# Kernel tuning notes

Hardware: AMD Instinct MI355X
Metric: run time of the kernel (lower is better)

## Reference

```python
import jax, jax.numpy as jnp
import numpy as np

B, S, D_IN, D_E = 8, 2048, 1024, 1024


def setup_inputs() -> dict:
    key = jax.random.key(0)
    ks = jax.random.split(key, 9)
    s_in = 1.0 / np.sqrt(D_IN)
    s_e = 1.0 / np.sqrt(D_E)
    return {
        "x": jax.random.normal(ks[0], (B, S, D_IN), dtype=jnp.float32),
        "Wq": jax.random.uniform(ks[1], (D_IN, D_E), jnp.float32, -s_in, s_in),
        "bq": jax.random.uniform(ks[2], (D_E,), jnp.float32, -s_in, s_in),
        "Wk": jax.random.uniform(ks[3], (D_IN, D_E), jnp.float32, -s_in, s_in),
        "bk": jax.random.uniform(ks[4], (D_E,), jnp.float32, -s_in, s_in),
        "Wv": jax.random.uniform(ks[5], (D_IN, D_E), jnp.float32, -s_in, s_in),
        "bv": jax.random.uniform(ks[6], (D_E,), jnp.float32, -s_in, s_in),
        "Wo": jax.random.uniform(ks[7], (D_E, D_E), jnp.float32, -s_e, s_e),
        "bo": jax.random.uniform(ks[8], (D_E,), jnp.float32, -s_e, s_e),
    }


def reference(x, Wq, bq, Wk, bk, Wv, bv, Wo, bo):
    # QKV projections: [B,S,D_in] @ [D_in,D_e] -> [B,S,D_e]
    Q = jnp.einsum("bsi,ie->bse", x, Wq) + bq
    K = jnp.einsum("bsi,ie->bse", x, Wk) + bk
    V = jnp.einsum("bsi,ie->bse", x, Wv) + bv
    scale = 1.0 / jnp.sqrt(jnp.asarray(Q.shape[-1], Q.dtype))
    # full score matrix [B,S,S] (faithful to the unfused original)
    logits = jnp.einsum("bqe,bke->bqk", Q, K) * scale
    attn = jax.nn.softmax(logits, axis=-1)
    values = jnp.einsum("bqk,bke->bqe", attn, V)
    o = jnp.einsum("bqe,ef->bqf", values, Wo) + bo
    return o
```

## Files before the change

### kernel.cpp

```cpp
#include <hip/hip_runtime.h>

#define DIN 1024
#define DE  1024
#define SEQ 2048
#define NB  8

typedef __bf16 bf16x8 __attribute__((ext_vector_type(8)));
typedef float  f32x4  __attribute__((ext_vector_type(4)));
typedef unsigned short u16;
typedef u16 u16x8 __attribute__((ext_vector_type(8)));
typedef u16 u16x4 __attribute__((ext_vector_type(4)));

__device__ __forceinline__ u16 f2bf(float f) {
  unsigned u = __builtin_bit_cast(unsigned, f);
  return (u16)((u + 0x7FFFu + ((u >> 16) & 1u)) >> 16);
}
__device__ __forceinline__ float bf2f(u16 h) {
  return __builtin_bit_cast(float, (unsigned)h << 16);
}

typedef __attribute__((address_space(1))) const unsigned char g_u8;
typedef __attribute__((address_space(3))) unsigned char l_u8;
__device__ __forceinline__ void gload16(const void* g, void* l) {
  __builtin_amdgcn_global_load_lds((g_u8*)g, (l_u8*)l, 16, 0, 0);
}

__global__ __launch_bounds__(256) void cvt_f32_bf16(const float* __restrict__ in,
                                                    u16* __restrict__ out, int n4) {
  int i = blockIdx.x * 256 + threadIdx.x;
  if (i >= n4) return;
  float4 v = ((const float4*)in)[i];
  u16x4 o;
  o[0] = f2bf(v.x); o[1] = f2bf(v.y); o[2] = f2bf(v.z); o[3] = f2bf(v.w);
  ((u16x4*)out)[i] = o;
}

__global__ __launch_bounds__(256) void transpose_w(const float* __restrict__ W,
                                                   u16* __restrict__ Wt) {
  __shared__ float t[32][33];
  const int tx = threadIdx.x, ty = threadIdx.y;
  const int bx = blockIdx.x * 32, by = blockIdx.y * 32;
#pragma unroll
  for (int i = 0; i < 4; ++i)
    t[ty + i * 8][tx] = W[(size_t)(by + ty + i * 8) * 1024 + bx + tx];
  __syncthreads();
#pragma unroll
  for (int i = 0; i < 4; ++i)
    Wt[(size_t)(bx + ty + i * 8) * 1024 + by + tx] = f2bf(t[tx][ty + i * 8]);
}

__global__ __launch_bounds__(256) void softmax_rows_bf16(u16* __restrict__ P) {
  const size_t row = blockIdx.x;
  u16* pr = P + row * 2048 + (size_t)threadIdx.x * 8;
  u16x8 v = *(const u16x8*)pr;
  float x[8];
#pragma unroll
  for (int j = 0; j < 8; ++j) x[j] = bf2f(v[j]);
  float m = x[0];
#pragma unroll
  for (int j = 1; j < 8; ++j) m = fmaxf(m, x[j]);
#pragma unroll
  for (int off = 32; off; off >>= 1) m = fmaxf(m, __shfl_xor(m, off));
  __shared__ float rm[4], rs[4];
  const int lane = threadIdx.x & 63, wid = threadIdx.x >> 6;
  if (lane == 0) rm[wid] = m;
  __syncthreads();
  m = fmaxf(fmaxf(rm[0], rm[1]), fmaxf(rm[2], rm[3]));
  float s = 0.f;
#pragma unroll
  for (int j = 0; j < 8; ++j) { x[j] = __expf(x[j] - m); s += x[j]; }
#pragma unroll
  for (int off = 32; off; off >>= 1) s += __shfl_xor(s, off);
  if (lane == 0) rs[wid] = s;
  __syncthreads();
  s = (rs[0] + rs[1]) + (rs[2] + rs[3]);
  const float inv = 1.f / s;
  u16x8 o;
#pragma unroll
  for (int j = 0; j < 8; ++j) o[j] = f2bf(x[j] * inv);
  *(u16x8*)pr = o;
}

template <int BMT, int OMODE, bool HAS_BIAS>
__global__ __launch_bounds__(512, 1) void gemmph(
    const u16* __restrict__ A, const u16* __restrict__ Bt, void* __restrict__ Cv,
    const float* __restrict__ bias, int M, int N, int K,
    size_t sA, size_t sB, size_t sC, float scale) {
  constexpr int ABYTES = BMT * 128;
  constexpr int AHALF  = ABYTES / 2;
  constexpr int BUFB   = ABYTES + 32768;
  constexpr int LA     = AHALF / 8192;
  constexpr int MR     = BMT / 32;
  __shared__ __align__(16) char lds8[2 * BUFB];
  const int tid = threadIdx.x, lane = tid & 63, wid = tid >> 6;
  const int wm = wid >> 2, wn = wid & 3;
  const int lane15 = lane & 15, gk = lane >> 4;

  const int gx = gridDim.x, gy = gridDim.y;
  int lin = blockIdx.x + gx * (blockIdx.y + gy * blockIdx.z);
  const int nwg = gx * gy * (int)gridDim.z;
  const int q = nwg >> 3, r8 = nwg & 7;
  const int xcd = lin & 7, idx = lin >> 3;
  lin = (xcd < r8 ? xcd * (q + 1) : r8 * (q + 1) + (xcd - r8) * q) + idx;
  const int bz = lin / (gx * gy);
  const int rem = lin - bz * (gx * gy);
  const int by = rem / gx, bx = rem - (rem / gx) * gx;

  const char* Ag = (const char*)(A + (size_t)bz * sA + (size_t)by * BMT * K);
  const char* Bg = (const char*)(Bt + (size_t)bz * sB + (size_t)bx * 256 * K);
  const size_t Kb = (size_t)K * 2;

  const int spr = tid >> 3;
  const int sg = (tid & 7) ^ (spr & 7);
  const char* srcA[2][2];
  const char* srcB[2][2];
#pragma unroll
  for (int h = 0; h < 2; ++h) {
#pragma unroll
    for (int j = 0; j < LA; ++j)
      srcA[h][j] = Ag + (size_t)(h * (BMT / 2) + j * 64 + spr) * Kb + sg * 16;
#pragma unroll
    for (int j = 0; j < 2; ++j)
      srcB[h][j] = Bg + (size_t)(h * 128 + j * 64 + spr) * Kb + sg * 16;
  }

  auto stageA2 = [&](int dbuf) {
#pragma unroll
    for (int h = 0; h < 2; ++h) {
      char* d = lds8 + dbuf * BUFB + h * AHALF + tid * 16;
#pragma unroll
      for (int j = 0; j < LA; ++j) { gload16(srcA[h][j], d + j * 8192); srcA[h][j] += 128; }
    }
  };
  auto stageB1 = [&](int h, int dbuf) {
    char* d = lds8 + dbuf * BUFB + ABYTES + h * 16384 + tid * 16;
    gload16(srcB[h][0], d);        srcB[h][0] += 128;
    gload16(srcB[h][1], d + 8192); srcB[h][1] += 128;
  };

  const int arow = lane15 * 128 + ((gk ^ (lane15 & 7)) << 4);

  f32x4 acc[MR][4] = {};
  const int NT = K >> 6;

  stageA2(0); stageB1(0, 0); stageB1(1, 0);
  stageB1(0, 1); stageA2(1);
  if constexpr (BMT == 256) asm volatile("s_waitcnt vmcnt(6)" ::: "memory");
  else                      asm volatile("s_waitcnt vmcnt(4)" ::: "memory");
  __builtin_amdgcn_s_barrier();
  __builtin_amdgcn_sched_barrier(0);

  for (int kt = 0; kt < NT; ++kt) {
    const char* Ab = lds8 + (kt & 1) * BUFB + wm * AHALF;
    const char* Bb = lds8 + (kt & 1) * BUFB + ABYTES + (wn >> 1) * 16384 + (wn & 1) * 8192;
    const int nbuf = (kt + 1) & 1;
    const int cbuf = kt & 1;
    bf16x8 af[4][2], bfr[4][2];

    if constexpr (BMT == 256) {
#pragma unroll
      for (int m = 0; m < 4; ++m) {
        af[m][0] = *(const bf16x8*)(Ab + m * 2048 + arow);
        af[m][1] = *(const bf16x8*)(Ab + m * 2048 + (arow ^ 64));
      }
#pragma unroll
      for (int n = 0; n < 2; ++n) {
        bfr[n][0] = *(const bf16x8*)(Bb + n * 2048 + arow);
        bfr[n][1] = *(const bf16x8*)(Bb + n * 2048 + (arow ^ 64));
      }
      if (kt + 1 < NT) stageB1(1, nbuf);
      __builtin_amdgcn_s_barrier();
      asm volatile("s_waitcnt lgkmcnt(0)" ::: "memory");
      __builtin_amdgcn_sched_barrier(0);
      __builtin_amdgcn_s_setprio(1);
#pragma unroll
      for (int m = 0; m < 4; ++m)
#pragma unroll
        for (int n = 0; n < 2; ++n) {
          acc[m][n] = __builtin_amdgcn_mfma_f32_16x16x32_bf16(af[m][0], bfr[n][0], acc[m][n], 0, 0, 0);
          acc[m][n] = __builtin_amdgcn_mfma_f32_16x16x32_bf16(af[m][1], bfr[n][1], acc[m][n], 0, 0, 0);
        }
      __builtin_amdgcn_s_setprio(0);
      __builtin_amdgcn_s_barrier();
      __builtin_amdgcn_sched_barrier(0);
#pragma unroll
      for (int n = 2; n < 4; ++n) {
        bfr[n][0] = *(const bf16x8*)(Bb + n * 2048 + arow);
        bfr[n][1] = *(const bf16x8*)(Bb + n * 2048 + (arow ^ 64));
      }
      __builtin_amdgcn_s_barrier();
      asm volatile("s_waitcnt lgkmcnt(0)" ::: "memory");
      __builtin_amdgcn_sched_barrier(0);
      __builtin_amdgcn_s_setprio(1);
#pragma unroll
      for (int m = 0; m < 4; ++m)
#pragma unroll
        for (int n = 2; n < 4; ++n) {
          acc[m][n] = __builtin_amdgcn_mfma_f32_16x16x32_bf16(af[m][0], bfr[n][0], acc[m][n], 0, 0, 0);
          acc[m][n] = __builtin_amdgcn_mfma_f32_16x16x32_bf16(af[m][1], bfr[n][1], acc[m][n], 0, 0, 0);
        }
      __builtin_amdgcn_s_setprio(0);
      __builtin_amdgcn_s_barrier();
      __builtin_amdgcn_sched_barrier(0);
#pragma unroll
      for (int m = 0; m < 4; ++m) {
        af[m][0] = *(const bf16x8*)(Ab + (4 + m) * 2048 + arow);
        af[m][1] = *(const bf16x8*)(Ab + (4 + m) * 2048 + (arow ^ 64));
      }
      if (kt + 2 < NT) stageB1(0, cbuf);
      __builtin_amdgcn_s_barrier();
      asm volatile("s_waitcnt lgkmcnt(0)" ::: "memory");
      __builtin_amdgcn_sched_barrier(0);
      __builtin_amdgcn_s_setprio(1);
#pragma unroll
      for (int m = 0; m < 4; ++m)
#pragma unroll
        for (int n = 0; n < 2; ++n) {
          acc[4 + m][n] = __builtin_amdgcn_mfma_f32_16x16x32_bf16(af[m][0], bfr[n][0], acc[4 + m][n], 0, 0, 0);
          acc[4 + m][n] = __builtin_amdgcn_mfma_f32_16x16x32_bf16(af[m][1], bfr[n][1], acc[4 + m][n], 0, 0, 0);
        }
      __builtin_amdgcn_s_setprio(0);
      __builtin_amdgcn_s_barrier();
      __builtin_amdgcn_sched_barrier(0);
      if (kt + 2 < NT) stageA2(cbuf);
      __builtin_amdgcn_s_barrier();
      asm volatile("s_waitcnt lgkmcnt(0)" ::: "memory");
      __builtin_amdgcn_sched_barrier(0);
      __builtin_amdgcn_s_setprio(1);
#pragma unroll
      for (int m = 0; m < 4; ++m)
#pragma unroll
        for (int n = 2; n < 4; ++n) {
          acc[4 + m][n] = __builtin_amdgcn_mfma_f32_16x16x32_bf16(af[m][0], bfr[n][0], acc[4 + m][n], 0, 0, 0);
          acc[4 + m][n] = __builtin_amdgcn_mfma_f32_16x16x32_bf16(af[m][1], bfr[n][1], acc[4 + m][n], 0, 0, 0);
        }
      __builtin_amdgcn_s_setprio(0);
      if (kt < NT - 2)      asm volatile("s_waitcnt vmcnt(6)" ::: "memory");
      else if (kt == NT - 2) asm volatile("s_waitcnt vmcnt(0)" ::: "memory");
      __builtin_amdgcn_s_barrier();
      __builtin_amdgcn_sched_barrier(0);
    } else {
#pragma unroll
      for (int m = 0; m < 4; ++m) {
        af[m][0] = *(const bf16x8*)(Ab + m * 2048 + arow);
        af[m][1] = *(const bf16x8*)(Ab + m * 2048 + (arow ^ 64));
      }
#pragma unroll
      for (int n = 0; n < 4; ++n) {
        bfr[n][0] = *(const bf16x8*)(Bb + n * 2048 + arow);
        bfr[n][1] = *(const bf16x8*)(Bb + n * 2048 + (arow ^ 64));
      }
      if (kt + 1 < NT) stageB1(1, nbuf);
      __builtin_amdgcn_s_barrier();
      asm volatile("s_waitcnt lgkmcnt(0)" ::: "memory");
      __builtin_amdgcn_sched_barrier(0);
      __builtin_amdgcn_s_setprio(1);
#pragma unroll
      for (int m = 0; m < 4; ++m)
#pragma unroll
        for (int n = 0; n < 2; ++n) {
          acc[m][n] = __builtin_amdgcn_mfma_f32_16x16x32_bf16(af[m][0], bfr[n][0], acc[m][n], 0, 0, 0);
          acc[m][n] = __builtin_amdgcn_mfma_f32_16x16x32_bf16(af[m][1], bfr[n][1], acc[m][n], 0, 0, 0);
        }
      __builtin_amdgcn_s_setprio(0);
      __builtin_amdgcn_s_barrier();
      __builtin_amdgcn_sched_barrier(0);
      if (kt + 2 < NT) { stageA2(cbuf); stageB1(0, cbuf); }
      __builtin_amdgcn_s_barrier();
      asm volatile("s_waitcnt lgkmcnt(0)" ::: "memory");
      __builtin_amdgcn_sched_barrier(0);
      __builtin_amdgcn_s_setprio(1);
#pragma unroll
      for (int m = 0; m < 4; ++m)
#pragma unroll
        for (int n = 2; n < 4; ++n) {
          acc[m][n] = __builtin_amdgcn_mfma_f32_16x16x32_bf16(af[m][0], bfr[n][0], acc[m][n], 0, 0, 0);
          acc[m][n] = __builtin_amdgcn_mfma_f32_16x16x32_bf16(af[m][1], bfr[n][1], acc[m][n], 0, 0, 0);
        }
      __builtin_amdgcn_s_setprio(0);
      if (kt < NT - 2)      asm volatile("s_waitcnt vmcnt(4)" ::: "memory");
      else if (kt == NT - 2) asm volatile("s_waitcnt vmcnt(0)" ::: "memory");
      __builtin_amdgcn_s_barrier();
      __builtin_amdgcn_sched_barrier(0);
    }
  }

  const int rbase = by * BMT + wm * (BMT / 2) + (gk << 2);
  const int cbase = bx * 256 + wn * 64 + lane15;
#pragma unroll
  for (int m = 0; m < MR; ++m)
#pragma unroll
    for (int n = 0; n < 4; ++n) {
      const int col = cbase + n * 16;
      const float bval = HAS_BIAS ? bias[col] : 0.f;
#pragma unroll
      for (int r = 0; r < 4; ++r) {
        const int rowg = rbase + m * 16 + r;
        const float v = acc[m][n][r] * scale + bval;
        if (OMODE == 0)
          ((float*)Cv)[(size_t)bz * sC + (size_t)rowg * N + col] = v;
        else if (OMODE == 1)
          ((u16*)Cv)[(size_t)bz * sC + (size_t)rowg * N + col] = f2bf(v);
        else
          ((u16*)Cv)[(size_t)(rowg >> 11) * ((size_t)DE * SEQ) +
                     (size_t)col * SEQ + (rowg & 2047)] = f2bf(v);
      }
    }
}

extern "C" void kernel_launch(void* const* d_in, const int* in_sizes, int n_in,
                              void* d_out, int out_size, void* d_ws, size_t ws_size,
                              hipStream_t stream) {
  const float* x  = (const float*)d_in[0];
  const float* Wq = (const float*)d_in[1];
  const float* bq = (const float*)d_in[2];
  const float* Wk = (const float*)d_in[3];
  const float* bk = (const float*)d_in[4];
  const float* Wv = (const float*)d_in[5];
  const float* bv = (const float*)d_in[6];
  const float* Wo = (const float*)d_in[7];
  const float* bo = (const float*)d_in[8];

  const size_t NEED = 142606336;
  if (ws_size < NEED) return;
  char* ws = (char*)d_ws;
  u16* x_bf = (u16*)(ws);
  u16* q_bf = (u16*)(ws + 33554432);
  u16* k_bf = (u16*)(ws + 67108864);
  u16* vt   = (u16*)(ws + 100663296);
  u16* wt   = (u16*)(ws + 134217728);
  u16* lgP  = (u16*)d_out;
  u16* wt_q = wt;
  u16* wt_k = wt + 1048576;
  u16* wt_v = wt + 2097152;
  u16* wt_o = wt + 3145728;

  dim3 tb(32, 8);
  const size_t sQ = (size_t)SEQ * DE;
  const size_t sL = (size_t)SEQ * SEQ;

  cvt_f32_bf16<<<16384, 256, 0, stream>>>(x, x_bf, (NB * SEQ * DIN) / 4);
  transpose_w<<<dim3(32, 32), tb, 0, stream>>>(Wq, wt_q);
  transpose_w<<<dim3(32, 32), tb, 0, stream>>>(Wk, wt_k);
  transpose_w<<<dim3(32, 32), tb, 0, stream>>>(Wv, wt_v);
  transpose_w<<<dim3(32, 32), tb, 0, stream>>>(Wo, wt_o);
  gemmph<256, 1, true><<<dim3(4, 64, 1), 512, 0, stream>>>(x_bf, wt_q, q_bf, bq,
      16384, 1024, 1024, 0, 0, 0, 1.f);
  gemmph<256, 1, true><<<dim3(4, 64, 1), 512, 0, stream>>>(x_bf, wt_k, k_bf, bk,
      16384, 1024, 1024, 0, 0, 0, 1.f);
  gemmph<256, 2, true><<<dim3(4, 64, 1), 512, 0, stream>>>(x_bf, wt_v, vt, bv,
      16384, 1024, 1024, 0, 0, 0, 1.f);
  gemmph<256, 1, false><<<dim3(8, 8, 8), 512, 0, stream>>>(q_bf, k_bf, lgP,
      nullptr, 2048, 2048, 1024, sQ, sQ, sL, 0.03125f);
  softmax_rows_bf16<<<16384, 256, 0, stream>>>(lgP);
  gemmph<256, 1, false><<<dim3(4, 8, 8), 512, 0, stream>>>(lgP, vt, q_bf,
      nullptr, 2048, 1024, 2048, sL, sQ, sQ, 1.f);
  gemmph<256, 0, true><<<dim3(4, 64, 1), 512, 0, stream>>>(q_bf, wt_o, d_out, bo,
      16384, 1024, 1024, 0, 0, 0, 1.f);

  (void)in_sizes; (void)n_in; (void)out_size; (void)ws_size;
}
```

Before: 334.6 us.

## Add 256x128-tile batched GEMM kernel for attention score and PV products

```diff
diff --git a/kernel.cpp b/kernel.cpp
--- a/kernel.cpp
+++ b/kernel.cpp
@@ -79,6 +79,98 @@
 #pragma unroll
   for (int j = 0; j < 8; ++j) o[j] = f2bf(x[j] * inv);
   *(u16x8*)pr = o;
+}
+
+__global__ __launch_bounds__(256) void gemmcc(
+    const u16* __restrict__ A, const u16* __restrict__ Bt, u16* __restrict__ C,
+    int M, int N, int K, size_t sA, size_t sB, size_t sC, float scale) {
+  constexpr int BUF = 24576;
+  __shared__ __align__(16) char lds[2 * BUF];
+  const int tid = threadIdx.x, lane = tid & 63, wid = tid >> 6;
+  const int wm = wid >> 1, wn = wid & 1;
+  const int lane15 = lane & 15, gk = lane >> 4;
+
+  const int gx = gridDim.x, gy = gridDim.y;
+  int lin = blockIdx.x + gx * (blockIdx.y + gy * blockIdx.z);
+  const int nwg = gx * gy * (int)gridDim.z;
+  const int q = nwg >> 3, r8 = nwg & 7;
+  const int xcd = lin & 7, idx = lin >> 3;
+  lin = (xcd < r8 ? xcd * (q + 1) : r8 * (q + 1) + (xcd - r8) * q) + idx;
+  const int bz = lin / (gx * gy);
+  const int rem = lin - bz * (gx * gy);
+  const int by = rem / gx, bx = rem - (rem / gx) * gx;
+
+  const char* Ag = (const char*)(A + (size_t)bz * sA + (size_t)by * 256 * K);
+  const char* Bg = (const char*)(Bt + (size_t)bz * sB + (size_t)bx * 128 * K);
+  const size_t Kb = (size_t)K * 2;
+
+  const char* sa[4];
+  const char* sb[2];
+  int dA[4], dB[2];
+#pragma unroll
+  for (int j = 0; j < 4; ++j) {
+    const int ls = j * 256 + tid, pr = ls >> 2, ps = ls & 3;
+    sa[j] = Ag + (size_t)pr * Kb + (ps ^ ((pr >> 1) & 3)) * 16;
+    dA[j] = ls * 16;
+  }
+#pragma unroll
+  for (int j = 0; j < 2; ++j) {
+    const int ls = j * 256 + tid, pr = ls >> 2, ps = ls & 3;
+    sb[j] = Bg + (size_t)pr * Kb + (ps ^ ((pr >> 1) & 3)) * 16;
+    dB[j] = 16384 + ls * 16;
+  }
+  auto stage = [&](int b) {
+    char* base = lds + b * BUF;
+#pragma unroll
+    for (int j = 0; j < 4; ++j) { gload16(sa[j], base + dA[j]); sa[j] += 64; }
+#pragma unroll
+    for (int j = 0; j < 2; ++j) { gload16(sb[j], base + dB[j]); sb[j] += 64; }
+  };
+
+  const int sw = (gk ^ ((lane15 >> 1) & 3)) << 4;
+  const int aoffB = wm * 8192 + lane15 * 64 + sw;
+  const int boffB = 16384 + wn * 4096 + lane15 * 64 + sw;
+
+  f32x4 acc[8][4] = {};
+  const int NT = K >> 5;
+
+  stage(0);
+  asm volatile("s_waitcnt vmcnt(0)" ::: "memory");
+  __builtin_amdgcn_s_barrier();
+  __builtin_amdgcn_sched_barrier(0);
+
+  for (int t = 0; t < NT; ++t) {
+    if (t + 1 < NT) stage((t + 1) & 1);
+    const char* base = lds + (t & 1) * BUF;
+    bf16x8 af[8], bfv[4];
+#pragma unroll
+    for (int n = 0; n < 4; ++n) bfv[n] = *(const bf16x8*)(base + boffB + n * 1024);
+#pragma unroll
+    for (int m = 0; m < 8; ++m) af[m] = *(const bf16x8*)(base + aoffB + m * 1024);
+    __builtin_amdgcn_s_setprio(1);
+#pragma unroll
+    for (int m = 0; m < 8; ++m)
+#pragma unroll
+      for (int n = 0; n < 4; ++n)
+        acc[m][n] = __builtin_amdgcn_mfma_f32_16x16x32_bf16(af[m], bfv[n], acc[m][n], 0, 0, 0);
+    __builtin_amdgcn_s_setprio(0);
+    asm volatile("s_waitcnt vmcnt(0)" ::: "memory");
+    __builtin_amdgcn_s_barrier();
+    __builtin_amdgcn_sched_barrier(0);
+  }
+
+  const int rbase = by * 256 + wm * 128 + (gk << 2);
+  const int cbase = bx * 128 + wn * 64 + lane15;
+  u16* Cb = C + (size_t)bz * sC;
+#pragma unroll
+  for (int m = 0; m < 8; ++m)
+#pragma unroll
+    for (int n = 0; n < 4; ++n) {
+      const int col = cbase + n * 16;
+#pragma unroll
+      for (int r = 0; r < 4; ++r)
+        Cb[(size_t)(rbase + m * 16 + r) * N + col] = f2bf(acc[m][n][r] * scale);
+    }
 }
 
 template <int BMT, int OMODE, bool HAS_BIAS>
@@ -145,8 +237,7 @@
 
   stageA2(0); stageB1(0, 0); stageB1(1, 0);
   stageB1(0, 1); stageA2(1);
-  if constexpr (BMT == 256) asm volatile("s_waitcnt vmcnt(6)" ::: "memory");
-  else                      asm volatile("s_waitcnt vmcnt(4)" ::: "memory");
+  asm volatile("s_waitcnt vmcnt(6)" ::: "memory");
   __builtin_amdgcn_s_barrier();
   __builtin_amdgcn_sched_barrier(0);
 
@@ -157,132 +248,87 @@
     const int cbuf = kt & 1;
     bf16x8 af[4][2], bfr[4][2];
 
-    if constexpr (BMT == 256) {
-#pragma unroll
-      for (int m = 0; m < 4; ++m) {
-        af[m][0] = *(const bf16x8*)(Ab + m * 2048 + arow);
-        af[m][1] = *(const bf16x8*)(Ab + m * 2048 + (arow ^ 64));
+#pragma unroll
+    for (int m = 0; m < 4; ++m) {
+      af[m][0] = *(const bf16x8*)(Ab + m * 2048 + arow);
+      af[m][1] = *(const bf16x8*)(Ab + m * 2048 + (arow ^ 64));
+    }
+#pragma unroll
+    for (int n = 0; n < 2; ++n) {
+      bfr[n][0] = *(const bf16x8*)(Bb + n * 2048 + arow);
+      bfr[n][1] = *(const bf16x8*)(Bb + n * 2048 + (arow ^ 64));
+    }
+    if (kt + 1 < NT) stageB1(1, nbuf);
+    __builtin_amdgcn_s_barrier();
+    asm volatile("s_waitcnt lgkmcnt(0)" ::: "memory");
+    __builtin_amdgcn_sched_barrier(0);
+    __builtin_amdgcn_s_setprio(1);
+#pragma unroll
+    for (int m = 0; m < 4; ++m)
+#pragma unroll
+      for (int n = 0; n < 2; ++n) {
+        acc[m][n] = __builtin_amdgcn_mfma_f32_16x16x32_bf16(af[m][0], bfr[n][0], acc[m][n], 0, 0, 0);
+        acc[m][n] = __builtin_amdgcn_mfma_f32_16x16x32_bf16(af[m][1], bfr[n][1], acc[m][n], 0, 0, 0);
       }
+    __builtin_amdgcn_s_setprio(0);
+    __builtin_amdgcn_s_barrier();
+    __builtin_amdgcn_sched_barrier(0);
+#pragma unroll
+    for (int n = 2; n < 4; ++n) {
+      bfr[n][0] = *(const bf16x8*)(Bb + n * 2048 + arow);
+      bfr[n][1] = *(const bf16x8*)(Bb + n * 2048 + (arow ^ 64));
+    }
+    __builtin_amdgcn_s_barrier();
+    asm volatile("s_waitcnt lgkmcnt(0)" ::: "memory");
+    __builtin_amdgcn_sched_barrier(0);
+    __builtin_amdgcn_s_setprio(1);
+#pragma unroll
+    for (int m = 0; m < 4; ++m)
+#pragma unroll
+      for (int n = 2; n < 4; ++n) {
+        acc[m][n] = __builtin_amdgcn_mfma_f32_16x16x32_bf16(af[m][0], bfr[n][0], acc[m][n], 0, 0, 0);
+        acc[m][n] = __builtin_amdgcn_mfma_f32_16x16x32_bf16(af[m][1], bfr[n][1], acc[m][n], 0, 0, 0);
+      }
+    __builtin_amdgcn_s_setprio(0);
+    __builtin_amdgcn_s_barrier();
+    __builtin_amdgcn_sched_barrier(0);
+#pragma unroll
+    for (int m = 0; m < 4; ++m) {
+      af[m][0] = *(const bf16x8*)(Ab + (4 + m) * 2048 + arow);
+      af[m][1] = *(const bf16x8*)(Ab + (4 + m) * 2048 + (arow ^ 64));
+    }
+    if (kt + 2 < NT) stageB1(0, cbuf);
+    __builtin_amdgcn_s_barrier();
+    asm volatile("s_waitcnt lgkmcnt(0)" ::: "memory");
+    __builtin_amdgcn_sched_barrier(0);
+    __builtin_amdgcn_s_setprio(1);
+#pragma unroll
+    for (int m = 0; m < 4; ++m)
 #pragma unroll
       for (int n = 0; n < 2; ++n) {
-        bfr[n][0] = *(const bf16x8*)(Bb + n * 2048 + arow);
-        bfr[n][1] = *(const bf16x8*)(Bb + n * 2048 + (arow ^ 64));
+        acc[4 + m][n] = __builtin_amdgcn_mfma_f32_16x16x32_bf16(af[m][0], bfr[n][0], acc[4 + m][n], 0, 0, 0);
+        acc[4 + m][n] = __builtin_amdgcn_mfma_f32_16x16x32_bf16(af[m][1], bfr[n][1], acc[4 + m][n], 0, 0, 0);
       }
-      if (kt + 1 < NT) stageB1(1, nbuf);
-      __builtin_amdgcn_s_barrier();
-      asm volatile("s_waitcnt lgkmcnt(0)" ::: "memory");
-      __builtin_amdgcn_sched_barrier(0);
-      __builtin_amdgcn_s_setprio(1);
-#pragma unroll
-      for (int m = 0; m < 4; ++m)
-#pragma unroll
-        for (int n = 0; n < 2; ++n) {
-          acc[m][n] = __builtin_amdgcn_mfma_f32_16x16x32_bf16(af[m][0], bfr[n][0], acc[m][n], 0, 0, 0);
-          acc[m][n] = __builtin_amdgcn_mfma_f32_16x16x32_bf16(af[m][1], bfr[n][1], acc[m][n], 0, 0, 0);
-        }
-      __builtin_amdgcn_s_setprio(0);
-      __builtin_amdgcn_s_barrier();
-      __builtin_amdgcn_sched_barrier(0);
+    __builtin_amdgcn_s_setprio(0);
+    __builtin_amdgcn_s_barrier();
+    __builtin_amdgcn_sched_barrier(0);
+    if (kt + 2 < NT) stageA2(cbuf);
+    __builtin_amdgcn_s_barrier();
+    asm volatile("s_waitcnt lgkmcnt(0)" ::: "memory");
+    __builtin_amdgcn_sched_barrier(0);
+    __builtin_amdgcn_s_setprio(1);
+#pragma unroll
+    for (int m = 0; m < 4; ++m)
 #pragma unroll
       for (int n = 2; n < 4; ++n) {
-        bfr[n][0] = *(const bf16x8*)(Bb + n * 2048 + arow);
-        bfr[n][1] = *(const bf16x8*)(Bb + n * 2048 + (arow ^ 64));
+        acc[4 + m][n] = __builtin_amdgcn_mfma_f32_16x16x32_bf16(af[m][0], bfr[n][0], acc[4 + m][n], 0, 0, 0);
+        acc[4 + m][n] = __builtin_amdgcn_mfma_f32_16x16x32_bf16(af[m][1], bfr[n][1], acc[4 + m][n], 0, 0, 0);
       }
-      __builtin_amdgcn_s_barrier();
-      asm volatile("s_waitcnt lgkmcnt(0)" ::: "memory");
-      __builtin_amdgcn_sched_barrier(0);
-      __builtin_amdgcn_s_setprio(1);
-#pragma unroll
-      for (int m = 0; m < 4; ++m)
-#pragma unroll
-        for (int n = 2; n < 4; ++n) {
-          acc[m][n] = __builtin_amdgcn_mfma_f32_16x16x32_bf16(af[m][0], bfr[n][0], acc[m][n], 0, 0, 0);
-          acc[m][n] = __builtin_amdgcn_mfma_f32_16x16x32_bf16(af[m][1], bfr[n][1], acc[m][n], 0, 0, 0);
-        }
-      __builtin_amdgcn_s_setprio(0);
-      __builtin_amdgcn_s_barrier();
-      __builtin_amdgcn_sched_barrier(0);
-#pragma unroll
-      for (int m = 0; m < 4; ++m) {
-        af[m][0] = *(const bf16x8*)(Ab + (4 + m) * 2048 + arow);
-        af[m][1] = *(const bf16x8*)(Ab + (4 + m) * 2048 + (arow ^ 64));
-      }
-      if (kt + 2 < NT) stageB1(0, cbuf);
-      __builtin_amdgcn_s_barrier();
-      asm volatile("s_waitcnt lgkmcnt(0)" ::: "memory");
-      __builtin_amdgcn_sched_barrier(0);
-      __builtin_amdgcn_s_setprio(1);
-#pragma unroll
-      for (int m = 0; m < 4; ++m)
-#pragma unroll
-        for (int n = 0; n < 2; ++n) {
-          acc[4 + m][n] = __builtin_amdgcn_mfma_f32_16x16x32_bf16(af[m][0], bfr[n][0], acc[4 + m][n], 0, 0, 0);
-          acc[4 + m][n] = __builtin_amdgcn_mfma_f32_16x16x32_bf16(af[m][1], bfr[n][1], acc[4 + m][n], 0, 0, 0);
-        }
-      __builtin_amdgcn_s_setprio(0);
-      __builtin_amdgcn_s_barrier();
-      __builtin_amdgcn_sched_barrier(0);
-      if (kt + 2 < NT) stageA2(cbuf);
-      __builtin_amdgcn_s_barrier();
-      asm volatile("s_waitcnt lgkmcnt(0)" ::: "memory");
-      __builtin_amdgcn_sched_barrier(0);
-      __builtin_amdgcn_s_setprio(1);
-#pragma unroll
-      for (int m = 0; m < 4; ++m)
-#pragma unroll
-        for (int n = 2; n < 4; ++n) {
-          acc[4 + m][n] = __builtin_amdgcn_mfma_f32_16x16x32_bf16(af[m][0], bfr[n][0], acc[4 + m][n], 0, 0, 0);
-          acc[4 + m][n] = __builtin_amdgcn_mfma_f32_16x16x32_bf16(af[m][1], bfr[n][1], acc[4 + m][n], 0, 0, 0);
-        }
-      __builtin_amdgcn_s_setprio(0);
-      if (kt < NT - 2)      asm volatile("s_waitcnt vmcnt(6)" ::: "memory");
-      else if (kt == NT - 2) asm volatile("s_waitcnt vmcnt(0)" ::: "memory");
-      __builtin_amdgcn_s_barrier();
-      __builtin_amdgcn_sched_barrier(0);
-    } else {
-#pragma unroll
-      for (int m = 0; m < 4; ++m) {
-        af[m][0] = *(const bf16x8*)(Ab + m * 2048 + arow);
-        af[m][1] = *(const bf16x8*)(Ab + m * 2048 + (arow ^ 64));
-      }
-#pragma unroll
-      for (int n = 0; n < 4; ++n) {
-        bfr[n][0] = *(const bf16x8*)(Bb + n * 2048 + arow);
-        bfr[n][1] = *(const bf16x8*)(Bb + n * 2048 + (arow ^ 64));
-      }
-      if (kt + 1 < NT) stageB1(1, nbuf);
-      __builtin_amdgcn_s_barrier();
-      asm volatile("s_waitcnt lgkmcnt(0)" ::: "memory");
-      __builtin_amdgcn_sched_barrier(0);
-      __builtin_amdgcn_s_setprio(1);
-#pragma unroll
-      for (int m = 0; m < 4; ++m)
-#pragma unroll
-        for (int n = 0; n < 2; ++n) {
-          acc[m][n] = __builtin_amdgcn_mfma_f32_16x16x32_bf16(af[m][0], bfr[n][0], acc[m][n], 0, 0, 0);
-          acc[m][n] = __builtin_amdgcn_mfma_f32_16x16x32_bf16(af[m][1], bfr[n][1], acc[m][n], 0, 0, 0);
-        }
-      __builtin_amdgcn_s_setprio(0);
-      __builtin_amdgcn_s_barrier();
-      __builtin_amdgcn_sched_barrier(0);
-      if (kt + 2 < NT) { stageA2(cbuf); stageB1(0, cbuf); }
-      __builtin_amdgcn_s_barrier();
-      asm volatile("s_waitcnt lgkmcnt(0)" ::: "memory");
-      __builtin_amdgcn_sched_barrier(0);
-      __builtin_amdgcn_s_setprio(1);
-#pragma unroll
-      for (int m = 0; m < 4; ++m)
-#pragma unroll
-        for (int n = 2; n < 4; ++n) {
-          acc[m][n] = __builtin_amdgcn_mfma_f32_16x16x32_bf16(af[m][0], bfr[n][0], acc[m][n], 0, 0, 0);
-          acc[m][n] = __builtin_amdgcn_mfma_f32_16x16x32_bf16(af[m][1], bfr[n][1], acc[m][n], 0, 0, 0);
-        }
-      __builtin_amdgcn_s_setprio(0);
-      if (kt < NT - 2)      asm volatile("s_waitcnt vmcnt(4)" ::: "memory");
-      else if (kt == NT - 2) asm volatile("s_waitcnt vmcnt(0)" ::: "memory");
-      __builtin_amdgcn_s_barrier();
-      __builtin_amdgcn_sched_barrier(0);
-    }
+    __builtin_amdgcn_s_setprio(0);
+    if (kt < NT - 2)      asm volatile("s_waitcnt vmcnt(6)" ::: "memory");
+    else if (kt == NT - 2) asm volatile("s_waitcnt vmcnt(0)" ::: "memory");
+    __builtin_amdgcn_s_barrier();
+    __builtin_amdgcn_sched_barrier(0);
   }
 
   const int rbase = by * BMT + wm * (BMT / 2) + (gk << 2);
@@ -350,11 +396,11 @@
       16384, 1024, 1024, 0, 0, 0, 1.f);
   gemmph<256, 2, true><<<dim3(4, 64, 1), 512, 0, stream>>>(x_bf, wt_v, vt, bv,
       16384, 1024, 1024, 0, 0, 0, 1.f);
-  gemmph<256, 1, false><<<dim3(8, 8, 8), 512, 0, stream>>>(q_bf, k_bf, lgP,
-      nullptr, 2048, 2048, 1024, sQ, sQ, sL, 0.03125f);
+  gemmcc<<<dim3(16, 8, 8), 256, 0, stream>>>(q_bf, k_bf, lgP,
+      2048, 2048, 1024, sQ, sQ, sL, 0.03125f);
   softmax_rows_bf16<<<16384, 256, 0, stream>>>(lgP);
-  gemmph<256, 1, false><<<dim3(4, 8, 8), 512, 0, stream>>>(lgP, vt, q_bf,
-      nullptr, 2048, 1024, 2048, sL, sQ, sQ, 1.f);
+  gemmcc<<<dim3(8, 8, 8), 256, 0, stream>>>(lgP, vt, q_bf,
+      2048, 1024, 2048, sL, sQ, sQ, 1.f);
   gemmph<256, 0, true><<<dim3(4, 64, 1), 512, 0, stream>>>(q_bf, wt_o, d_out, bo,
       16384, 1024, 1024, 0, 0, 0, 1.f);
 
```

Measured after the change: 391.6 us. +17.0%, slower.
